# Kernel optimization log

Hardware: AMD Instinct MI355X
Metric: run time of the kernel (lower is better)

Reference implementation:

```python
import jax, jax.numpy as jnp
import numpy as np

SR = 44100
K = 1.0 / SR                      # time step
LX = 0.5
MAX_OM = 10000.0 * 2.0 * np.pi    # fmax * 2pi
MIN_OM = 20.0 * 2.0 * np.pi
TAU0, TAU1 = 6.0, 1.0
OM2SQ = (2.0 * np.pi * 500.0) ** 2          # OmDamp2^2 (OmDamp1 = 0)
ALPHA = 3.0 * np.log(10.0) / OM2SQ * (OM2SQ / TAU0)   # = 3 ln10 / tau0
BETA = 3.0 * np.log(10.0) / OM2SQ * (1.0 / TAU1 - 1.0 / TAU0)
MU_SCALE, DMU_SCALE, T0MU_SCALE = 2.43, 0.002452, 0.004115
M_MAX = 80  # 80x80 = 6400 modes


def setup_inputs() -> dict:
    z = jnp.zeros((), dtype=jnp.float32)
    return {
        "mu_raw": z, "D_over_mu_raw": z, "T0_over_mu_raw": z,
        "Ly_raw": z, "xo_raw": z, "yo_raw": z,
        "num_samples": 22050,
    }


def _modal_ir(mu_raw, D_over_mu_raw, T0_over_mu_raw, Ly_raw, xo_raw, yo_raw, num_samples):
    sp, sg = jax.nn.softplus, jax.nn.sigmoid
    # physical parameters via differentiable bounds
    mu = (sp(mu_raw) + 1e-4) * MU_SCALE
    D_over_mu = (sp(D_over_mu_raw) + 1e-4) * DMU_SCALE
    T0_over_mu = (sp(T0_over_mu_raw) + 1e-4) * T0MU_SCALE
    Ly = 1.1 + (4.0 - 1.1) * sg(Ly_raw)
    xo = 0.49 * LX + (1.0 - 0.49) * LX * sg(xo_raw)
    yo = 0.51 * Ly + (1.0 - 0.51) * Ly * sg(yo_raw)
    xi = 0.1 * LX
    yi = 0.1 * Ly
    # mode grid [6400]
    idx = jnp.arange(1, M_MAX + 1, dtype=jnp.float32)
    gm, gn = jnp.meshgrid(idx, idx, indexing="ij")
    m, n = gm.ravel(), gn.ravel()
    g1 = (m * np.pi / LX) ** 2 + (n * np.pi / Ly) ** 2
    omega_sq = T0_over_mu * g1 + D_over_mu * g1 * g1
    omega = jnp.sqrt(jax.nn.relu(omega_sq))
    valid = ((omega <= MAX_OM) & (omega >= MIN_OM)).astype(omega.dtype)
    InW = jnp.cos(xi * np.pi * m / LX) * jnp.cos(yi * np.pi * n / Ly)
    OutW = jnp.cos(xo * np.pi * m / LX) * jnp.cos(yo * np.pi * n / Ly)
    sigma = ALPHA + BETA * omega ** 2
    ms = 0.25 * mu * LX * Ly
    P = OutW * InW * (K * K) * jnp.exp(-sigma * K) / ms * valid  # [modes]
    # time axis [T]
    t = jnp.arange(num_samples, dtype=jnp.float32)
    decay_env = jnp.exp(-sigma[:, None] * (t[None, :] - 1.0) * K)    # [modes, T]
    sine_num = jnp.sin(t[None, :] * omega[:, None] * K)              # [modes, T]
    sine_den = jnp.sin(omega * K) + 1e-8                             # [modes]
    mode_waveforms = P[:, None] * decay_env * (sine_num / sine_den[:, None])
    disp = jnp.sum(mode_waveforms, axis=0)                           # [T]
    peak = jnp.max(jnp.abs(disp)) + 1e-8
    return disp / peak


def reference(mu_raw, D_over_mu_raw, T0_over_mu_raw, Ly_raw, xo_raw, yo_raw, num_samples):
    return _modal_ir(mu_raw, D_over_mu_raw, T0_over_mu_raw, Ly_raw, xo_raw, yo_raw, num_samples)
```

## Files before the change

### kernel.cpp

```cpp
#include <hip/hip_runtime.h>
#include <math.h>

#define NMODES 6400
#define TB     128
#define MPT    10
#define NPAIR  5
#define MG     5
#define BATCH  6
#define TC     42
#define NORMB  256

typedef float v2f __attribute__((ext_vector_type(2)));

static __device__ __forceinline__ float softplusf(float x) {
    return log1pf(expf(-fabsf(x))) + fmaxf(x, 0.0f);
}
static __device__ __forceinline__ float sigmoidf(float x) {
    return 1.0f / (1.0f + expf(-x));
}

__global__ void setup_zero_kernel(const float* __restrict__ mu_raw,
                                  const float* __restrict__ Dmu_raw,
                                  const float* __restrict__ T0mu_raw,
                                  const float* __restrict__ Ly_raw,
                                  const float* __restrict__ xo_raw,
                                  const float* __restrict__ yo_raw,
                                  float* __restrict__ wsA,
                                  float* __restrict__ wsW,
                                  float* __restrict__ wsS,
                                  float* __restrict__ wsCW,
                                  float* __restrict__ wsSW,
                                  unsigned int* __restrict__ peak,
                                  unsigned int* __restrict__ done,
                                  float* __restrict__ out, int T)
{
    int id = blockIdx.x * blockDim.x + threadIdx.x;
    int gsz = gridDim.x * blockDim.x;
    for (int i = id; i < T; i += gsz) out[i] = 0.0f;
    if (id == 0) { *peak = 0u; *done = 0u; }
    if (id >= NMODES) return;

    const float KF   = 1.0f / 44100.0f;
    const float PI_F = (float)M_PI;
    const double om2sq = (2.0 * M_PI * 500.0) * (2.0 * M_PI * 500.0);
    const float ALPHA_F  = (float)(3.0 * M_LN10 / om2sq * (om2sq / 6.0));
    const float BETA_F   = (float)(3.0 * M_LN10 / om2sq * (1.0 - 1.0 / 6.0));
    const float MAX_OM_F = (float)(10000.0 * 2.0 * M_PI);
    const float MIN_OM_F = (float)(20.0 * 2.0 * M_PI);
    const float KK_F     = (float)((1.0 / 44100.0) * (1.0 / 44100.0));

    float mu   = (softplusf(mu_raw[0])   + 1e-4f) * 2.43f;
    float Dmu  = (softplusf(Dmu_raw[0])  + 1e-4f) * 0.002452f;
    float T0mu = (softplusf(T0mu_raw[0]) + 1e-4f) * 0.004115f;
    float Ly   = 1.1f + 2.9f * sigmoidf(Ly_raw[0]);
    float xo   = 0.245f + 0.255f * sigmoidf(xo_raw[0]);
    float yo   = __fadd_rn(__fmul_rn(0.51f, Ly),
                           __fmul_rn(__fmul_rn(0.49f, Ly), sigmoidf(yo_raw[0])));

    float mf = (float)(id / 80 + 1);
    float nf = (float)(id % 80 + 1);

    float am = __fmul_rn(__fmul_rn(mf, PI_F), 2.0f);
    float bn = __fdiv_rn(__fmul_rn(nf, PI_F), Ly);
    float g1 = __fadd_rn(__fmul_rn(am, am), __fmul_rn(bn, bn));
    float omega_sq = __fadd_rn(__fmul_rn(T0mu, g1),
                               __fmul_rn(__fmul_rn(Dmu, g1), g1));
    float omega = sqrtf(fmaxf(omega_sq, 0.0f));
    float valid = (omega <= MAX_OM_F && omega >= MIN_OM_F) ? 1.0f : 0.0f;

    float xi_pi = (float)(0.05 * M_PI);
    float yi = __fmul_rn(0.1f, Ly);
    float InW = __fmul_rn(
        cosf(__fmul_rn(__fmul_rn(xi_pi, mf), 2.0f)),
        cosf(__fdiv_rn(__fmul_rn(__fmul_rn(yi, PI_F), nf), Ly)));
    float OutW = __fmul_rn(
        cosf(__fmul_rn(__fmul_rn(__fmul_rn(xo, PI_F), mf), 2.0f)),
        cosf(__fdiv_rn(__fmul_rn(__fmul_rn(yo, PI_F), nf), Ly)));

    float sigma = __fadd_rn(ALPHA_F, __fmul_rn(BETA_F, __fmul_rn(omega, omega)));
    float ms = __fmul_rn(__fmul_rn(__fmul_rn(0.25f, mu), 0.5f), Ly);
    float P = __fmul_rn(
        __fdiv_rn(__fmul_rn(__fmul_rn(__fmul_rn(OutW, InW), KK_F),
                            expf(__fmul_rn(-sigma, KF))),
                  ms),
        valid);
    float den = __fadd_rn(sinf(__fmul_rn(omega, KF)), 1e-8f);
    float A = __fdiv_rn(P, den);

    const double Kd = 1.0 / 44100.0;
    double th = (double)omega * Kd;
    double dd = exp(-(double)sigma * Kd);
    wsA[id]  = A;
    wsW[id]  = omega;
    wsS[id]  = sigma;
    wsCW[id] = (float)(dd * cos(th));
    wsSW[id] = (float)(dd * sin(th));
}

__global__ __launch_bounds__(TB) void accum_kernel(
    const float* __restrict__ wsA,
    const float* __restrict__ wsW,
    const float* __restrict__ wsS,
    const float* __restrict__ wsCW,
    const float* __restrict__ wsSW,
    float* __restrict__ out, int T)
{
    __shared__ __align__(16) float lds[TC][TB + 2];

    const int tid  = threadIdx.x;
    const int t0   = blockIdx.x * TC;
    const int base = blockIdx.y * (TB * MPT);

    const float  KF     = 1.0f / 44100.0f;
    const double Kd     = 1.0 / 44100.0;
    const double TWO_PI = 6.283185307179586476925286766559;
    const double I2PI   = 0.15915494309189533576888376337251;

    v2f S[NPAIR], C[NPAIR], CW[NPAIR], SW[NPAIR];
    #pragma unroll
    for (int p = 0; p < NPAIR; ++p) {
        int m = base + p * (TB * 2) + tid * 2;
        CW[p] = *(const v2f*)(wsCW + m);
        SW[p] = *(const v2f*)(wsSW + m);
        v2f A  = *(const v2f*)(wsA + m);
        v2f w  = *(const v2f*)(wsW + m);
        v2f sg = *(const v2f*)(wsS + m);
        #pragma unroll
        for (int k = 0; k < 2; ++k) {
            double ph = (double)t0 * (double)w[k] * Kd;
            double q  = rint(ph * I2PI);
            float  r  = (float)fma(-q, TWO_PI, ph);
            float s0, c0;
            __sincosf(r, &s0, &c0);
            float env = A[k] * __expf(-sg[k] * (float)(t0 - 1) * KF);
            S[p][k] = env * s0;
            C[p][k] = env * c0;
        }
    }

    #pragma unroll 1
    for (int it = 0; it < TC; it += BATCH) {
        #pragma unroll
        for (int b = 0; b < BATCH; ++b) {
            v2f s01 = S[0] + S[1];
            v2f s23 = S[2] + S[3];
            v2f sp  = (s01 + s23) + S[4];
            lds[it + b][tid] = sp[0] + sp[1];
            #pragma unroll
            for (int p = 0; p < NPAIR; ++p) {
                v2f nS = __builtin_elementwise_fma(S[p], CW[p], C[p] * SW[p]);
                v2f nC = __builtin_elementwise_fma(C[p], CW[p], -(S[p] * SW[p]));
                S[p] = nS;
                C[p] = nC;
            }
        }
    }
    __syncthreads();

    const int wv   = tid >> 6;
    const int lane = tid & 63;
    if (lane < TC / 2) {
        int s = wv * (TC / 2) + lane;
        v2f z = {0.0f, 0.0f};
        #pragma unroll
        for (int r = 0; r < TB / 2; ++r)
            z += *(const v2f*)&lds[s][2 * r];
        int t = t0 + s;
        if (t < T) atomicAdd(&out[t], z[0] + z[1]);
    }
}

__global__ __launch_bounds__(NORMB) void norm_kernel(
    float* __restrict__ out,
    unsigned int* peak,
    unsigned int* done, int T, int nblk)
{
    __shared__ float red[NORMB / 64];
    __shared__ float pks;

    int i = blockIdx.x * NORMB + threadIdx.x;
    v2f v = {0.0f, 0.0f};
    bool full = (2 * i + 1 < T), half = (!full && 2 * i < T);
    if (full)      v = *(const v2f*)(out + 2 * i);
    else if (half) v[0] = out[2 * i];

    float mx = fmaxf(fabsf(v[0]), fabsf(v[1]));
    #pragma unroll
    for (int off = 32; off > 0; off >>= 1)
        mx = fmaxf(mx, __shfl_xor(mx, off, 64));
    int lane = threadIdx.x & 63, wv = threadIdx.x >> 6;
    if (lane == 0) red[wv] = mx;
    __syncthreads();

    if (threadIdx.x == 0) {
        float m = red[0];
        #pragma unroll
        for (int k = 1; k < NORMB / 64; ++k) m = fmaxf(m, red[k]);
        atomicMax(peak, __float_as_uint(m));
        __hip_atomic_fetch_add(done, 1u, __ATOMIC_RELEASE,
                               __HIP_MEMORY_SCOPE_AGENT);
        unsigned int x;
        do {
            __builtin_amdgcn_s_sleep(2);
            x = __hip_atomic_load(done, __ATOMIC_ACQUIRE,
                                  __HIP_MEMORY_SCOPE_AGENT);
        } while (x < (unsigned int)nblk);
        pks = __uint_as_float(__hip_atomic_load(peak, __ATOMIC_RELAXED,
                                                __HIP_MEMORY_SCOPE_AGENT)) + 1e-8f;
    }
    __syncthreads();

    float pk = pks;
    if (full) {
        v[0] = __fdiv_rn(v[0], pk);
        v[1] = __fdiv_rn(v[1], pk);
        *(v2f*)(out + 2 * i) = v;
    } else if (half) {
        out[2 * i] = __fdiv_rn(v[0], pk);
    }
}

extern "C" void kernel_launch(void* const* d_in, const int* in_sizes, int n_in,
                              void* d_out, int out_size, void* d_ws, size_t ws_size,
                              hipStream_t stream)
{
    const float* mu   = (const float*)d_in[0];
    const float* Dmu  = (const float*)d_in[1];
    const float* T0mu = (const float*)d_in[2];
    const float* Lyr  = (const float*)d_in[3];
    const float* xor_ = (const float*)d_in[4];
    const float* yor_ = (const float*)d_in[5];
    float* out = (float*)d_out;

    float* ws   = (float*)d_ws;
    float* wsA  = ws;
    float* wsW  = ws + NMODES;
    float* wsS  = ws + 2 * NMODES;
    float* wsCW = ws + 3 * NMODES;
    float* wsSW = ws + 4 * NMODES;
    unsigned int* peak = (unsigned int*)(ws + 5 * NMODES);
    unsigned int* done = (unsigned int*)(ws + 5 * NMODES + 1);

    int T = out_size;
    int tchunks = (T + TC - 1) / TC;
    int npairs  = (T + 1) / 2;
    int nblk    = (npairs + NORMB - 1) / NORMB;

    setup_zero_kernel<<<(NMODES + 255) / 256, 256, 0, stream>>>(
        mu, Dmu, T0mu, Lyr, xor_, yor_, wsA, wsW, wsS, wsCW, wsSW,
        peak, done, out, T);
    accum_kernel<<<dim3(tchunks, MG), TB, 0, stream>>>(
        wsA, wsW, wsS, wsCW, wsSW, out, T);
    norm_kernel<<<nblk, NORMB, 0, stream>>>(out, peak, done, T, nblk);
}
```

Measured before the change: 91.51 us.

## Replace atomic accumulation with per-mode-group partial buffers reduced in norm kernel

```diff
diff --git a/kernel.cpp b/kernel.cpp
--- a/kernel.cpp
+++ b/kernel.cpp
@@ -6,8 +6,10 @@
 #define MPT    10
 #define NPAIR  5
 #define MG     5
-#define BATCH  6
 #define TC     42
+#define TCH    21
+#define BATCH  7
+#define PSTRIDE 22080
 #define NORMB  256
 
 typedef float v2f __attribute__((ext_vector_type(2)));
@@ -19,24 +21,21 @@
     return 1.0f / (1.0f + expf(-x));
 }
 
-__global__ void setup_zero_kernel(const float* __restrict__ mu_raw,
-                                  const float* __restrict__ Dmu_raw,
-                                  const float* __restrict__ T0mu_raw,
-                                  const float* __restrict__ Ly_raw,
-                                  const float* __restrict__ xo_raw,
-                                  const float* __restrict__ yo_raw,
-                                  float* __restrict__ wsA,
-                                  float* __restrict__ wsW,
-                                  float* __restrict__ wsS,
-                                  float* __restrict__ wsCW,
-                                  float* __restrict__ wsSW,
-                                  unsigned int* __restrict__ peak,
-                                  unsigned int* __restrict__ done,
-                                  float* __restrict__ out, int T)
+__global__ void setup_kernel(const float* __restrict__ mu_raw,
+                             const float* __restrict__ Dmu_raw,
+                             const float* __restrict__ T0mu_raw,
+                             const float* __restrict__ Ly_raw,
+                             const float* __restrict__ xo_raw,
+                             const float* __restrict__ yo_raw,
+                             float* __restrict__ wsA,
+                             float* __restrict__ wsW,
+                             float* __restrict__ wsS,
+                             float* __restrict__ wsCW,
+                             float* __restrict__ wsSW,
+                             unsigned int* __restrict__ peak,
+                             unsigned int* __restrict__ done)
 {
     int id = blockIdx.x * blockDim.x + threadIdx.x;
-    int gsz = gridDim.x * blockDim.x;
-    for (int i = id; i < T; i += gsz) out[i] = 0.0f;
     if (id == 0) { *peak = 0u; *done = 0u; }
     if (id >= NMODES) return;
 
@@ -103,13 +102,15 @@
     const float* __restrict__ wsS,
     const float* __restrict__ wsCW,
     const float* __restrict__ wsSW,
-    float* __restrict__ out, int T)
-{
-    __shared__ __align__(16) float lds[TC][TB + 2];
+    float* __restrict__ part, int T)
+{
+    __shared__ __align__(16) float lds[TCH][TB + 2];
 
     const int tid  = threadIdx.x;
     const int t0   = blockIdx.x * TC;
     const int base = blockIdx.y * (TB * MPT);
+    const int wv   = tid >> 6;
+    const int lane = tid & 63;
 
     const float  KF     = 1.0f / 44100.0f;
     const double Kd     = 1.0 / 44100.0;
@@ -138,39 +139,45 @@
         }
     }
 
+    const int  o   = (wv == 0) ? lane : (11 + lane);
+    const bool own = (wv == 0) ? (lane < 11) : (lane < 10);
+
     #pragma unroll 1
-    for (int it = 0; it < TC; it += BATCH) {
-        #pragma unroll
-        for (int b = 0; b < BATCH; ++b) {
-            v2f s01 = S[0] + S[1];
-            v2f s23 = S[2] + S[3];
-            v2f sp  = (s01 + s23) + S[4];
-            lds[it + b][tid] = sp[0] + sp[1];
+    for (int ph2 = 0; ph2 < 2; ++ph2) {
+        #pragma unroll 1
+        for (int it = 0; it < TCH; it += BATCH) {
             #pragma unroll
-            for (int p = 0; p < NPAIR; ++p) {
-                v2f nS = __builtin_elementwise_fma(S[p], CW[p], C[p] * SW[p]);
-                v2f nC = __builtin_elementwise_fma(C[p], CW[p], -(S[p] * SW[p]));
-                S[p] = nS;
-                C[p] = nC;
+            for (int b = 0; b < BATCH; ++b) {
+                v2f s01 = S[0] + S[1];
+                v2f s23 = S[2] + S[3];
+                v2f sp  = (s01 + s23) + S[4];
+                lds[it + b][tid] = sp[0] + sp[1];
+                #pragma unroll
+                for (int p = 0; p < NPAIR; ++p) {
+                    v2f nS = __builtin_elementwise_fma(S[p], CW[p], C[p] * SW[p]);
+                    v2f nC = __builtin_elementwise_fma(C[p], CW[p], -(S[p] * SW[p]));
+                    S[p] = nS;
+                    C[p] = nC;
+                }
             }
         }
-    }
-    __syncthreads();
-
-    const int wv   = tid >> 6;
-    const int lane = tid & 63;
-    if (lane < TC / 2) {
-        int s = wv * (TC / 2) + lane;
-        v2f z = {0.0f, 0.0f};
-        #pragma unroll
-        for (int r = 0; r < TB / 2; ++r)
-            z += *(const v2f*)&lds[s][2 * r];
-        int t = t0 + s;
-        if (t < T) atomicAdd(&out[t], z[0] + z[1]);
+        __syncthreads();
+
+        if (own) {
+            v2f z = {0.0f, 0.0f};
+            #pragma unroll
+            for (int r = 0; r < TB / 2; ++r)
+                z += *(const v2f*)&lds[o][2 * r];
+            int t = t0 + ph2 * TCH + o;
+            if (t < T)
+                part[blockIdx.y * PSTRIDE + t] = z[0] + z[1];
+        }
+        __syncthreads();
     }
 }
 
 __global__ __launch_bounds__(NORMB) void norm_kernel(
+    const float* __restrict__ part,
     float* __restrict__ out,
     unsigned int* peak,
     unsigned int* done, int T, int nblk)
@@ -181,8 +188,15 @@
     int i = blockIdx.x * NORMB + threadIdx.x;
     v2f v = {0.0f, 0.0f};
     bool full = (2 * i + 1 < T), half = (!full && 2 * i < T);
-    if (full)      v = *(const v2f*)(out + 2 * i);
-    else if (half) v[0] = out[2 * i];
+    if (full) {
+        #pragma unroll
+        for (int g = 0; g < MG; ++g)
+            v += *(const v2f*)(part + g * PSTRIDE + 2 * i);
+    } else if (half) {
+        #pragma unroll
+        for (int g = 0; g < MG; ++g)
+            v[0] += part[g * PSTRIDE + 2 * i];
+    }
 
     float mx = fmaxf(fabsf(v[0]), fabsf(v[1]));
     #pragma unroll
@@ -240,16 +254,16 @@
     float* wsSW = ws + 4 * NMODES;
     unsigned int* peak = (unsigned int*)(ws + 5 * NMODES);
     unsigned int* done = (unsigned int*)(ws + 5 * NMODES + 1);
+    float* part = ws + 5 * NMODES + 16;
 
     int T = out_size;
     int tchunks = (T + TC - 1) / TC;
     int npairs  = (T + 1) / 2;
     int nblk    = (npairs + NORMB - 1) / NORMB;
 
-    setup_zero_kernel<<<(NMODES + 255) / 256, 256, 0, stream>>>(
-        mu, Dmu, T0mu, Lyr, xor_, yor_, wsA, wsW, wsS, wsCW, wsSW,
-        peak, done, out, T);
+    setup_kernel<<<(NMODES + 255) / 256, 256, 0, stream>>>(
+        mu, Dmu, T0mu, Lyr, xor_, yor_, wsA, wsW, wsS, wsCW, wsSW, peak, done);
     accum_kernel<<<dim3(tchunks, MG), TB, 0, stream>>>(
-        wsA, wsW, wsS, wsCW, wsSW, out, T);
-    norm_kernel<<<nblk, NORMB, 0, stream>>>(out, peak, done, T, nblk);
-}
+        wsA, wsW, wsS, wsCW, wsSW, part, T);
+    norm_kernel<<<nblk, NORMB, 0, stream>>>(part, out, peak, done, T, nblk);
+}
```

Result: slower. 95.11 us (+3.9%).
